# Optimization experiments

Measured on AMD Instinct MI355X. Metric: run time of the kernel, lower is better.

## Reference

```python
import jax, jax.numpy as jnp
import numpy as np

H = 1024        # bridge_hidden_dim
NH = 16         # num_attention_heads
HD = H // NH    # head_dim = 64
B, S = 4, 1024
PHYS_W = 0.2
CONS_W = 0.15


def setup_inputs() -> dict:
    key = jax.random.key(0)
    ks = jax.random.split(key, 16)
    sc = 0.02
    return {
        "cnn_features": jax.random.normal(ks[0], (B, S, H), jnp.float32),
        "llm_features": jax.random.normal(ks[1], (B, S, H), jnp.float32),
        "Wq": jax.random.normal(ks[2], (H, H), jnp.float32) * sc,
        "bq": jnp.zeros((H,), jnp.float32),
        "Wk": jax.random.normal(ks[3], (H, H), jnp.float32) * sc,
        "bk": jnp.zeros((H,), jnp.float32),
        "Wv": jax.random.normal(ks[4], (H, H), jnp.float32) * sc,
        "bv": jnp.zeros((H,), jnp.float32),
        "Wo": jax.random.normal(ks[5], (H, H), jnp.float32) * sc,
        "bo": jnp.zeros((H,), jnp.float32),
        "ln_g": jnp.ones((H,), jnp.float32),
        "ln_b": jnp.zeros((H,), jnp.float32),
        "e_energy": jax.random.normal(ks[6], (H,), jnp.float32),
        "e_mass": jax.random.normal(ks[7], (H,), jnp.float32),
        "e_momentum": jax.random.normal(ks[8], (H,), jnp.float32),
    }


def _layernorm(x, g, b, eps=1e-5):
    mu = jnp.mean(x, axis=-1, keepdims=True)
    var = jnp.var(x, axis=-1, keepdims=True)
    return (x - mu) * jax.lax.rsqrt(var + eps) * g + b


def _split_heads(x):
    b, s, _ = x.shape
    return x.reshape(b, s, NH, HD).transpose(0, 2, 1, 3)  # [b, h, s, d]


def _physics_attention(q_in, k_in, v_in, Wq, bq, Wk, bk, Wv, bv, Wo, bo, ln_g, ln_b):
    # q_in: [b, sq, H]; k_in == v_in: [b, sk, H] with sq == sk (required by bias math)
    Q = _split_heads(q_in @ Wq.T + bq)  # [b,h,s,d]
    K = _split_heads(k_in @ Wk.T + bk)
    V = _split_heads(v_in @ Wv.T + bv)
    scores = jnp.einsum('bhqd,bhkd->bhqk', Q, K) / jnp.sqrt(jnp.float32(HD))
    # physics constraints (broadcast [b,h,s,1] over key axis)
    energy_bias = jnp.sum(Q * K, axis=-1, keepdims=True) * PHYS_W
    mass_bias = jnp.mean(Q + K, axis=-1, keepdims=True) * CONS_W
    scores = scores + energy_bias + mass_bias
    attn = jax.nn.softmax(scores, axis=-1)  # dropout is identity in eval
    att = jnp.einsum('bhqk,bhkd->bhqd', attn, V)
    b, h, s, d = att.shape
    att = att.transpose(0, 2, 1, 3).reshape(b, s, h * d)
    out = att @ Wo.T + bo
    return _layernorm(q_in + out, ln_g, ln_b)


def reference(cnn_features, llm_features, Wq, bq, Wk, bk, Wv, bv, Wo, bo,
              ln_g, ln_b, e_energy, e_mass, e_momentum):
    b = cnn_features.shape[0]
    phys = jnp.stack([e_energy, e_mass, e_momentum], axis=0)  # [3, H]
    phys = jnp.broadcast_to(phys[None], (b, 3, H))
    aug_cnn = jnp.concatenate([cnn_features, phys], axis=1)  # [b, S+3, H]
    aug_llm = jnp.concatenate([llm_features, phys], axis=1)
    cnn_att = _physics_attention(aug_cnn, aug_llm, aug_llm,
                                 Wq, bq, Wk, bk, Wv, bv, Wo, bo, ln_g, ln_b)
    llm_att = _physics_attention(aug_llm, aug_cnn, aug_cnn,
                                 Wq, bq, Wk, bk, Wv, bv, Wo, bo, ln_g, ln_b)
    cnn_out = cnn_att[:, :cnn_features.shape[1], :]
    llm_out = llm_att[:, :llm_features.shape[1], :]
    return (cnn_out, llm_out)
```

## Files before the change

kernel.cpp:

```cpp
#include <hip/hip_runtime.h>
#include <stdint.h>

#define SA 1027
#define SPAD 1088

typedef __attribute__((ext_vector_type(8))) short short8;
typedef __attribute__((ext_vector_type(4))) float f32x4;
typedef __attribute__((ext_vector_type(2))) unsigned int u32x2;

typedef const __attribute__((address_space(1))) uint8_t* gas1;
typedef __attribute__((address_space(3))) uint8_t* las3;

__device__ __forceinline__ void gload16(const void* g, void* l){
  __builtin_amdgcn_global_load_lds((gas1)g, (las3)l, 16, 0, 0);
}

__device__ __forceinline__ uint16_t f2bf(float f){
  uint32_t x = __builtin_bit_cast(uint32_t, f);
  x = (x + 0x7fffu + ((x >> 16) & 1u)) >> 16;
  return (uint16_t)x;
}
__device__ __forceinline__ float bf2f(uint16_t u){
  uint32_t x = ((uint32_t)u) << 16;
  return __builtin_bit_cast(float, x);
}

__device__ __forceinline__ f32x4 mfma16(short8 a, short8 b, f32x4 c){
  return __builtin_amdgcn_mfma_f32_16x16x32_bf16(a, b, c, 0, 0, 0);
}

#define QSCALE 0.18033688011112042f

__global__ __launch_bounds__(256) void prep_wb(
    const float* __restrict__ Wq, const float* __restrict__ Wk,
    const float* __restrict__ Wv, const float* __restrict__ Wo,
    const float* __restrict__ bq, const float* __restrict__ bk,
    const float* __restrict__ bv, const float* __restrict__ bo,
    uint16_t* __restrict__ W, float* __restrict__ bias){
  const int gid = blockIdx.x*256 + threadIdx.x;
  if (gid < 1048576){
    const int w = gid >> 18;
    const int off = (gid & 262143) << 2;
    const float* src = (w==0) ? Wq : (w==1) ? Wk : (w==2) ? Wv : Wo;
    const float4 v = *(const float4*)(src + off);
    ushort4 u;
    u.x = f2bf(v.x); u.y = f2bf(v.y); u.z = f2bf(v.z); u.w = f2bf(v.w);
    *(ushort4*)(W + ((size_t)w << 20) + off) = u;
  } else if (gid < 1048576 + 1024){
    const int i = (gid - 1048576) << 2;
    const int w = i >> 10;
    const int off = i & 1023;
    const float* src = (w==0) ? bq : (w==1) ? bk : (w==2) ? bv : bo;
    *(float4*)(bias + i) = *(const float4*)(src + off);
  }
}

__global__ __launch_bounds__(256) void prep_X(
    const float* __restrict__ cnn, const float* __restrict__ llm,
    uint16_t* __restrict__ X){
  const int row = blockIdx.x;
  const int c4 = threadIdx.x << 2;
  const int cb = row >> 10, s = row & 1023;
  const int c = cb >> 2, b = cb & 3;
  const float4 v = *(const float4*)((c ? llm : cnn) + ((size_t)(b*1024 + s))*1024 + c4);
  ushort4 u;
  u.x = f2bf(v.x); u.y = f2bf(v.y); u.z = f2bf(v.z); u.w = f2bf(v.w);
  *(ushort4*)(X + (size_t)row*1024 + c4) = u;
}

__global__ __launch_bounds__(256) void phys_qkv(
    const float* __restrict__ ee, const float* __restrict__ em,
    const float* __restrict__ ep, const uint16_t* __restrict__ W,
    const float* __restrict__ bias, uint16_t* __restrict__ Yqk,
    uint16_t* __restrict__ Vt){
  __shared__ float xs[1024];
  const int t = blockIdx.x >> 3;
  const int col = 1024 + (blockIdx.x & 7)*256 + threadIdx.x;
  const float* e = (t==0) ? ee : (t==1) ? em : ep;
  for (int k = threadIdx.x; k < 1024; k += 256) xs[k] = bf2f(f2bf(e[k]));
  __syncthreads();
  const uint16_t* wr = W + (size_t)col*1024;
  float acc = 0.f;
  for (int k = 0; k < 1024; k += 8){
    const short8 w8 = *(const short8*)(wr + k);
    #pragma unroll
    for (int u = 0; u < 8; ++u) acc += bf2f((uint16_t)w8[u]) * xs[k+u];
  }
  const uint16_t o = f2bf(acc + bias[col]);
  if (col < 2048){
    #pragma unroll
    for (int cb = 0; cb < 8; ++cb)
      Yqk[((size_t)cb*SA + 1024 + t)*2048 + col] = o;
  } else {
    const int hd = col - 2048;
    #pragma unroll
    for (int cb = 0; cb < 8; ++cb)
      Vt[((size_t)(cb*1024 + hd))*SPAD + 1024 + t] = o;
  }
}

__global__ __launch_bounds__(512) void qkv256(
    const uint16_t* __restrict__ A, const uint16_t* __restrict__ B,
    const float* __restrict__ bias, uint16_t* __restrict__ Yqk,
    uint16_t* __restrict__ Vt){
  extern __shared__ uint8_t lds[];
  const int tid = threadIdx.x;
  const int lane = tid & 63, wid = tid >> 6;
  const int l15 = lane & 15, l4 = lane >> 4;
  const int wm = wid >> 2, wn = wid & 3;
  const int wg = (blockIdx.x & 7)*48 + (blockIdx.x >> 3);
  const int bm = wg / 12, bn = wg % 12;

  const uint16_t* Ag = A + (size_t)bm*256*1024;
  const uint16_t* Bg = B + (size_t)bn*256*1024;

  const int srow8 = lane >> 3;
  const int gch = (lane & 7) ^ srow8;
  const int c0 = wid*2, c1 = c0 + 1;
  const size_t ga0 = (size_t)(c0*8 + srow8)*1024 + gch*8;
  const size_t ga1 = (size_t)(c1*8 + srow8)*1024 + gch*8;

#define STG_A(buf, H, kt) do { \
    gload16(Ag + (size_t)(H)*131072 + (size_t)(kt)*64 + ga0, lds + (buf)*65536 + (H)*16384 + c0*1024); \
    gload16(Ag + (size_t)(H)*131072 + (size_t)(kt)*64 + ga1, lds + (buf)*65536 + (H)*16384 + c1*1024); \
  } while(0)
#define STG_B(buf, H, kt) do { \
    gload16(Bg + (size_t)(H)*131072 + (size_t)(kt)*64 + ga0, lds + (buf)*65536 + 32768 + (H)*16384 + c0*1024); \
    gload16(Bg + (size_t)(H)*131072 + (size_t)(kt)*64 + ga1, lds + (buf)*65536 + 32768 + (H)*16384 + c1*1024); \
  } while(0)

  int koff[2];
  koff[0] = (l4*16) ^ ((l15 & 7) << 4);
  koff[1] = (64 + l4*16) ^ ((l15 & 7) << 4);
  const int arow = (wm*128 + l15) * 128;
  const int brow = (wn*64 + l15) * 128;

  f32x4 acc[8][4];
  #pragma unroll
  for (int i = 0; i < 8; ++i)
    #pragma unroll
    for (int j = 0; j < 4; ++j) acc[i][j] = (f32x4){0.f,0.f,0.f,0.f};

  const int NT = 16;
  STG_A(0,0,0); STG_A(0,1,0); STG_B(0,0,0); STG_B(0,1,0);
  STG_B(1,0,1); STG_B(1,1,1);
  asm volatile("s_waitcnt vmcnt(4)" ::: "memory");
  __builtin_amdgcn_s_barrier();

  for (int s = 0; s < NT; ++s){
    const int b = s & 1;
    const uint8_t* La = lds + b*65536;
    const uint8_t* Lb = La + 32768;
    const int sn1 = (s+1 < NT) ? s+1 : s;
    const int sn2 = (s+2 < NT) ? s+2 : s;
    const int nb = b ^ 1;
    short8 af[4][2], bf0[2][2], bf1[2][2];

    STG_A(nb, 0, sn1);
    #pragma unroll
    for (int i = 0; i < 4; ++i){
      af[i][0] = *(const short8*)(La + arow + i*2048 + koff[0]);
      af[i][1] = *(const short8*)(La + arow + i*2048 + koff[1]);
    }
    #pragma unroll
    for (int j = 0; j < 2; ++j){
      bf0[j][0] = *(const short8*)(Lb + brow + j*2048 + koff[0]);
      bf0[j][1] = *(const short8*)(Lb + brow + j*2048 + koff[1]);
    }
    __builtin_amdgcn_s_barrier();
    asm volatile("s_waitcnt lgkmcnt(0)" ::: "memory");
    __builtin_amdgcn_s_setprio(1);
    #pragma unroll
    for (int i = 0; i < 4; ++i)
      #pragma unroll
      for (int j = 0; j < 2; ++j)
        acc[i][j] = mfma16(af[i][1], bf0[j][1], mfma16(af[i][0], bf0[j][0], acc[i][j]));
    __builtin_amdgcn_s_setprio(0);
    __builtin_amdgcn_s_barrier();

    STG_A(nb, 1, sn1);
    #pragma unroll
    for (int j = 0; j < 2; ++j){
      bf1[j][0] = *(const short8*)(Lb + brow + (j+2)*2048 + koff[0]);
      bf1[j][1] = *(const short8*)(Lb + brow + (j+2)*2048 + koff[1]);
    }
    __builtin_amdgcn_s_barrier();
    asm volatile("s_waitcnt lgkmcnt(0)" ::: "memory");
    __builtin_amdgcn_s_setprio(1);
    #pragma unroll
    for (int i = 0; i < 4; ++i)
      #pragma unroll
      for (int j = 0; j < 2; ++j)
        acc[i][j+2] = mfma16(af[i][1], bf1[j][1], mfma16(af[i][0], bf1[j][0], acc[i][j+2]));
    __builtin_amdgcn_s_setprio(0);
    __builtin_amdgcn_s_barrier();

    STG_B(b, 0, sn2);
    #pragma unroll
    for (int i = 0; i < 4; ++i){
      af[i][0] = *(const short8*)(La + 8192 + arow + i*2048 + koff[0]);
      af[i][1] = *(const short8*)(La + 8192 + arow + i*2048 + koff[1]);
    }
    __builtin_amdgcn_s_barrier();
    asm volatile("s_waitcnt lgkmcnt(0)" ::: "memory");
    __builtin_amdgcn_s_setprio(1);
    #pragma unroll
    for (int i = 0; i < 4; ++i)
      #pragma unroll
      for (int j = 0; j < 2; ++j)
        acc[i+4][j+2] = mfma16(af[i][1], bf1[j][1], mfma16(af[i][0], bf1[j][0], acc[i+4][j+2]));
    __builtin_amdgcn_s_setprio(0);
    __builtin_amdgcn_s_barrier();

    STG_B(b, 1, sn2);
    __builtin_amdgcn_s_barrier();
    __builtin_amdgcn_s_setprio(1);
    #pragma unroll
    for (int i = 0; i < 4; ++i)
      #pragma unroll
      for (int j = 0; j < 2; ++j)
        acc[i+4][j] = mfma16(af[i][1], bf0[j][1], mfma16(af[i][0], bf0[j][0], acc[i+4][j]));
    __builtin_amdgcn_s_setprio(0);
    asm volatile("s_waitcnt vmcnt(4)" ::: "memory");
    __builtin_amdgcn_s_barrier();
  }

  #pragma unroll
  for (int j = 0; j < 4; ++j){
    const int n = bn*256 + wn*64 + j*16 + l15;
    const float bb = bias[n];
    if (n < 2048){
      const float sc = (n < 1024) ? QSCALE : 1.0f;
      #pragma unroll
      for (int i = 0; i < 8; ++i){
        const int m0 = bm*256 + wm*128 + i*16 + l4*4;
        #pragma unroll
        for (int r = 0; r < 4; ++r){
          const int m = m0 + r;
          Yqk[((size_t)(m >> 10)*SA + (m & 1023))*2048 + n] = f2bf((acc[i][j][r] + bb) * sc);
        }
      }
    } else {
      const int hd = n - 2048;
      #pragma unroll
      for (int i = 0; i < 8; ++i){
        const int m0 = bm*256 + wm*128 + i*16 + l4*4;
        const size_t vrow = (size_t)(m0 >> 10)*1024 + hd;
        const uint32_t w0 = (uint32_t)f2bf(acc[i][j][0] + bb) | ((uint32_t)f2bf(acc[i][j][1] + bb) << 16);
        const uint32_t w1 = (uint32_t)f2bf(acc[i][j][2] + bb) | ((uint32_t)f2bf(acc[i][j][3] + bb) << 16);
        *(u32x2*)(Vt + vrow*SPAD + (m0 & 1023)) = (u32x2){w0, w1};
      }
    }
  }
#undef STG_A
#undef STG_B
}

__global__ __launch_bounds__(512) void oproj256(
    const uint16_t* __restrict__ A, const uint16_t* __restrict__ B,
    const float* __restrict__ bias, uint16_t* __restrict__ C){
  extern __shared__ uint8_t lds[];
  const int tid = threadIdx.x;
  const int lane = tid & 63, wid = tid >> 6;
  const int l15 = lane & 15, l4 = lane >> 4;
  const int wm = wid >> 2, wn = wid & 3;
  const int wg = (blockIdx.x & 7)*32 + (blockIdx.x >> 3);
  const int bm = wg >> 3, bn = wg & 7;

  const uint16_t* Ag = A + (size_t)bm*256*1024;
  const uint16_t* Bg = B + (size_t)bn*128*1024;

  const int srow8 = lane >> 3;
  const int gch = (lane & 7) ^ srow8;
  const int c0 = wid*2, c1 = c0 + 1;
  const size_t ga0 = (size_t)(c0*8 + srow8)*1024 + gch*8;
  const size_t ga1 = (size_t)(c1*8 + srow8)*1024 + gch*8;

#define STG_A(buf, H, kt) do { \
    gload16(Ag + (size_t)(H)*131072 + (size_t)(kt)*64 + ga0, lds + (buf)*49152 + (H)*16384 + c0*1024); \
    gload16(Ag + (size_t)(H)*131072 + (size_t)(kt)*64 + ga1, lds + (buf)*49152 + (H)*16384 + c1*1024); \
  } while(0)
#define STG_B(buf, kt) do { \
    gload16(Bg + (size_t)(kt)*64 + ga0, lds + (buf)*49152 + 32768 + c0*1024); \
    gload16(Bg + (size_t)(kt)*64 + ga1, lds + (buf)*49152 + 32768 + c1*1024); \
  } while(0)

  int koff[2];
  koff[0] = (l4*16) ^ ((l15 & 7) << 4);
  koff[1] = (64 + l4*16) ^ ((l15 & 7) << 4);
  const int abase = wm*16384 + l15*128;
  const int bbase = 32768 + (wn*32 + l15)*128;

  f32x4 acc[8][2];
  #pragma unroll
  for (int i = 0; i < 8; ++i){ acc[i][0] = (f32x4){0,0,0,0}; acc[i][1] = (f32x4){0,0,0,0}; }

  const int NT = 16;
  STG_A(0,0,0); STG_A(0,1,0); STG_B(0,0); STG_B(1,1);
  asm volatile("s_waitcnt vmcnt(2)" ::: "memory");
  __builtin_amdgcn_s_barrier();

  for (int s = 0; s < NT; ++s){
    const int b = s & 1, nb = b ^ 1;
    const uint8_t* L = lds + b*49152;
    const int sn1 = (s+1 < NT) ? s+1 : s;
    const int sn2 = (s+2 < NT) ? s+2 : s;
    short8 af[4][2], bfr[2][2];

    STG_A(nb, 0, sn1);
    #pragma unroll
    for (int i = 0; i < 4; ++i){
      af[i][0] = *(const short8*)(L + abase + i*2048 + koff[0]);
      af[i][1] = *(const short8*)(L + abase + i*2048 + koff[1]);
    }
    #pragma unroll
    for (int j = 0; j < 2; ++j){
      bfr[j][0] = *(const short8*)(L + bbase + j*2048 + koff[0]);
      bfr[j][1] = *(const short8*)(L + bbase + j*2048 + koff[1]);
    }
    __builtin_amdgcn_s_barrier();
    asm volatile("s_waitcnt lgkmcnt(0)" ::: "memory");
    __builtin_amdgcn_s_setprio(1);
    #pragma unroll
    for (int i = 0; i < 4; ++i)
      #pragma unroll
      for (int j = 0; j < 2; ++j)
        acc[i][j] = mfma16(af[i][1], bfr[j][1], mfma16(af[i][0], bfr[j][0], acc[i][j]));
    __builtin_amdgcn_s_setprio(0);
    __builtin_amdgcn_s_barrier();

    STG_A(nb, 1, sn1);
    STG_B(b, sn2);
    #pragma unroll
    for (int i = 0; i < 4; ++i){
      af[i][0] = *(const short8*)(L + abase + 8192 + i*2048 + koff[0]);
      af[i][1] = *(const short8*)(L + abase + 8192 + i*2048 + koff[1]);
    }
    __builtin_amdgcn_s_barrier();
    asm volatile("s_waitcnt lgkmcnt(0)" ::: "memory");
    __builtin_amdgcn_s_setprio(1);
    #pragma unroll
    for (int i = 0; i < 4; ++i)
      #pragma unroll
      for (int j = 0; j < 2; ++j)
        acc[i+4][j] = mfma16(af[i][1], bfr[j][1], mfma16(af[i][0], bfr[j][0], acc[i+4][j]));
    __builtin_amdgcn_s_setprio(0);
    asm volatile("s_waitcnt vmcnt(2)" ::: "memory");
    __builtin_amdgcn_s_barrier();
  }

  #pragma unroll
  for (int j = 0; j < 2; ++j){
    const int n = bn*128 + wn*32 + j*16 + l15;
    const float bb = bias[n];
    #pragma unroll
    for (int i = 0; i < 8; ++i){
      const size_t m0 = (size_t)bm*256 + wm*128 + i*16 + l4*4;
      #pragma unroll
      for (int r = 0; r < 4; ++r)
        C[(m0 + r)*1024 + n] = f2bf(acc[i][j][r] + bb);
    }
  }
#undef STG_A
#undef STG_B
}

__global__ __launch_bounds__(512, 4) void attn_k(
    const uint16_t* __restrict__ Yqk, const uint16_t* __restrict__ Vt,
    uint16_t* __restrict__ att){
  __shared__ __align__(16) uint8_t smK[16384];
  __shared__ __align__(16) uint8_t smV[16384];
  __shared__ __align__(16) uint8_t smP[16384];
  const int tid = threadIdx.x;
  const int lane = tid & 63, wid = tid >> 6;
  const int l15 = lane & 15, l4 = lane >> 4;
  const int i = blockIdx.x;
  const int inst = (i & 7)*16 + ((i >> 3) & 15);
  const int qb = i >> 7;
  const int h = inst & 15, cb = inst >> 4;
  const size_t yrow0 = (size_t)cb * SA;
  const int q0 = qb*256 + wid*32;
  const size_t vbase = (size_t)inst * 64 * SPAD;
  const uint16_t* Yk = Yqk + yrow0*2048 + 1024 + h*64;

  short8 qf[2][2];
  #pragma unroll
  for (int u = 0; u < 2; ++u){
    const uint16_t* p = Yqk + (yrow0 + q0 + u*16 + l15)*2048 + h*64 + l4*8;
    qf[u][0] = *(const short8*)p;
    qf[u][1] = *(const short8*)(p + 32);
  }

  f32x4 o0[4], o1[4];
  float psum0 = 0.f, psum1 = 0.f;
  #pragma unroll
  for (int d = 0; d < 4; ++d){ o0[d] = (f32x4){0,0,0,0}; o1[d] = (f32x4){0,0,0,0}; }

  int koff[2], pwo[4];
  #pragma unroll
  for (int kk = 0; kk < 2; ++kk)
    koff[kk] = (l15*128 + kk*64 + l4*16) ^ ((l15 & 7) << 4);
  #pragma unroll
  for (int nt = 0; nt < 4; ++nt)
    pwo[nt] = (l15*128 + nt*32 + l4*8) ^ ((l15 & 7) << 4);
  uint8_t* const pb = smP + wid*2048;

  const int srow = lane >> 3, schunk = lane & 7;
  const int strow = wid*8 + srow;
  const int sgch = schunk ^ srow;
  {
    gload16(Yk + (size_t)strow*2048 + sgch*8, smK + wid*1024);
    gload16(Vt + vbase + (size_t)strow*SPAD + sgch*8, smV + wid*1024);
  }
  __syncthreads();

  int cur = 0;
  for (int kt = 0; kt < 17; ++kt){
    if (kt < 16){
      const int s1n = (kt + 1)*64;
      const int nb = (cur ^ 1)*8192;
      gload16(Yk + (size_t)(s1n + strow)*2048 + sgch*8, smK + nb + wid*1024);
      gload16(Vt + vbase + (size_t)strow*SPAD + s1n + sgch*8, smV + nb + wid*1024);
    }
    const uint8_t* bK = smK + cur*8192;
    const uint8_t* bV = smV + cur*8192;

    f32x4 sa[4], sb[4];
    #pragma unroll
    for (int nt = 0; nt < 4; ++nt){
      const short8 k0 = *(const short8*)(bK + nt*2048 + koff[0]);
      const short8 k1 = *(const short8*)(bK + nt*2048 + koff[1]);
      sa[nt] = mfma16(k1, qf[0][1], mfma16(k0, qf[0][0], (f32x4){0,0,0,0}));
      sb[nt] = mfma16(k1, qf[1][1], mfma16(k0, qf[1][0], (f32x4){0,0,0,0}));
    }
    if (kt == 16){
      #pragma unroll
      for (int nt = 0; nt < 4; ++nt)
        #pragma unroll
        for (int r = 0; r < 4; ++r){
          if (nt*16 + l4*4 + r >= 3){ sa[nt][r] = -3e38f; sb[nt][r] = -3e38f; }
        }
    }
    #pragma unroll
    for (int nt = 0; nt < 4; ++nt){
      const float p0 = __builtin_amdgcn_exp2f(sa[nt][0]);
      const float p1 = __builtin_amdgcn_exp2f(sa[nt][1]);
      const float p2 = __builtin_amdgcn_exp2f(sa[nt][2]);
      const float p3 = __builtin_amdgcn_exp2f(sa[nt][3]);
      psum0 += (p0 + p1) + (p2 + p3);
      uint32_t w0, w1;
      asm("v_cvt_pk_bf16_f32 %0, %1, %2" : "=v"(w0) : "v"(p0), "v"(p1));
      asm("v_cvt_pk_bf16_f32 %0, %1, %2" : "=v"(w1) : "v"(p2), "v"(p3));
      *(u32x2*)(pb + pwo[nt]) = (u32x2){w0, w1};
    }
    short8 vf[4][2];
    #pragma unroll
    for (int dt = 0; dt < 4; ++dt){
      vf[dt][0] = *(const short8*)(bV + dt*2048 + koff[0]);
      vf[dt][1] = *(const short8*)(bV + dt*2048 + koff[1]);
    }
    #pragma unroll
    for (int kk = 0; kk < 2; ++kk){
      const short8 pf = *(const short8*)(pb + koff[kk]);
      #pragma unroll
      for (int dt = 0; dt < 4; ++dt)
        o0[dt] = mfma16(pf, vf[dt][kk], o0[dt]);
    }
    #pragma unroll
    for (int nt = 0; nt < 4; ++nt){
      const float p0 = __builtin_amdgcn_exp2f(sb[nt][0]);
      const float p1 = __builtin_amdgcn_exp2f(sb[nt][1]);
      const float p2 = __builtin_amdgcn_exp2f(sb[nt][2]);
      const float p3 = __builtin_amdgcn_exp2f(sb[nt][3]);
      psum1 += (p0 + p1) + (p2 + p3);
      uint32_t w0, w1;
      asm("v_cvt_pk_bf16_f32 %0, %1, %2" : "=v"(w0) : "v"(p0), "v"(p1));
      asm("v_cvt_pk_bf16_f32 %0, %1, %2" : "=v"(w1) : "v"(p2), "v"(p3));
      *(u32x2*)(pb + pwo[nt]) = (u32x2){w0, w1};
    }
    #pragma unroll
    for (int kk = 0; kk < 2; ++kk){
      const short8 pf = *(const short8*)(pb + koff[kk]);
      #pragma unroll
      for (int dt = 0; dt < 4; ++dt)
        o1[dt] = mfma16(pf, vf[dt][kk], o1[dt]);
    }
    __syncthreads();
    cur ^= 1;
  }

  psum0 += __shfl_xor(psum0, 16); psum0 += __shfl_xor(psum0, 32);
  psum1 += __shfl_xor(psum1, 16); psum1 += __shfl_xor(psum1, 32);
  const size_t arow0 = (size_t)cb*1024 + q0;
  #pragma unroll
  for (int r = 0; r < 4; ++r){
    const float inv0 = 1.f / __shfl(psum0, l4*4 + r);
    const float inv1 = 1.f / __shfl(psum1, l4*4 + r);
    #pragma unroll
    for (int dt = 0; dt < 4; ++dt){
      att[(arow0 + l4*4 + r)*1024 + h*64 + dt*16 + l15] = f2bf(o0[dt][r] * inv0);
      att[(arow0 + 16 + l4*4 + r)*1024 + h*64 + dt*16 + l15] = f2bf(o1[dt][r] * inv1);
    }
  }
}

__global__ __launch_bounds__(256) void ln_out(
    const uint16_t* __restrict__ Op, const float* __restrict__ cnn,
    const float* __restrict__ llm, const float* __restrict__ g,
    const float* __restrict__ b, float* __restrict__ out){
  const int row = blockIdx.x;
  const int c = row >> 12, bq = row & 4095;
  const int tid = threadIdx.x;
  const ushort4 u = *(const ushort4*)(Op + (size_t)row*1024 + (tid<<2));
  const float4 rv = *(const float4*)((c ? llm : cnn) + (size_t)bq*1024 + (tid<<2));
  const float x0 = bf2f(u.x) + rv.x;
  const float x1 = bf2f(u.y) + rv.y;
  const float x2 = bf2f(u.z) + rv.z;
  const float x3 = bf2f(u.w) + rv.w;
  float s1 = x0+x1+x2+x3;
  float s2 = x0*x0+x1*x1+x2*x2+x3*x3;
  #pragma unroll
  for (int m=1;m<64;m<<=1){ s1 += __shfl_xor(s1,m); s2 += __shfl_xor(s2,m); }
  __shared__ float r1[4], r2[4];
  const int wid = tid >> 6, lane = tid & 63;
  if (lane == 0){ r1[wid] = s1; r2[wid] = s2; }
  __syncthreads();
  s1 = r1[0]+r1[1]+r1[2]+r1[3];
  s2 = r2[0]+r2[1]+r2[2]+r2[3];
  const float mu = s1 * 0.0009765625f;
  const float var = s2 * 0.0009765625f - mu*mu;
  const float rs = rsqrtf(var + 1e-5f);
  const float4 gv = *(const float4*)(g + (tid<<2));
  const float4 bv = *(const float4*)(b + (tid<<2));
  float4 ov;
  ov.x = (x0 - mu)*rs*gv.x + bv.x;
  ov.y = (x1 - mu)*rs*gv.y + bv.y;
  ov.z = (x2 - mu)*rs*gv.z + bv.z;
  ov.w = (x3 - mu)*rs*gv.w + bv.w;
  *(float4*)(out + ((size_t)c << 22) + (size_t)bq*1024 + (tid<<2)) = ov;
}

extern "C" void kernel_launch(void* const* d_in, const int* in_sizes, int n_in,
                              void* d_out, int out_size, void* d_ws, size_t ws_size,
                              hipStream_t stream){
  const float* cnn = (const float*)d_in[0];
  const float* llm = (const float*)d_in[1];
  const float* Wq  = (const float*)d_in[2];
  const float* bq  = (const float*)d_in[3];
  const float* Wk  = (const float*)d_in[4];
  const float* bk  = (const float*)d_in[5];
  const float* Wv  = (const float*)d_in[6];
  const float* bv  = (const float*)d_in[7];
  const float* Wo  = (const float*)d_in[8];
  const float* bo  = (const float*)d_in[9];
  const float* lng = (const float*)d_in[10];
  const float* lnb = (const float*)d_in[11];
  const float* ee  = (const float*)d_in[12];
  const float* em  = (const float*)d_in[13];
  const float* ep  = (const float*)d_in[14];

  uint8_t* ws = (uint8_t*)d_ws;
  uint16_t* X    = (uint16_t*)(ws + 0);
  uint16_t* W    = (uint16_t*)(ws + 16777216);
  float*    bias = (float*)   (ws + 25165824);
  uint16_t* Yqk  = (uint16_t*)(ws + 25182208);
  uint16_t* Vt   = (uint16_t*)(ws + 59785216);
  uint16_t* att  = X;
  uint16_t* Op   = Yqk;
  float* out = (float*)d_out;

  hipFuncSetAttribute((const void*)qkv256,
                      hipFuncAttributeMaxDynamicSharedMemorySize, 131072);
  hipFuncSetAttribute((const void*)oproj256,
                      hipFuncAttributeMaxDynamicSharedMemorySize, 98304);

  prep_wb<<<4100, 256, 0, stream>>>(Wq, Wk, Wv, Wo, bq, bk, bv, bo, W, bias);
  prep_X<<<8192, 256, 0, stream>>>(cnn, llm, X);
  phys_qkv<<<24, 256, 0, stream>>>(ee, em, ep, W, bias, Yqk, Vt);
  qkv256<<<384, 512, 131072, stream>>>(X, W, bias, Yqk, Vt);
  attn_k<<<512, 512, 0, stream>>>(Yqk, Vt, att);
  oproj256<<<256, 512, 98304, stream>>>(att, W + 3145728, bias + 3072, Op);
  ln_out<<<8192, 256, 0, stream>>>(Op, cnn, llm, lng, lnb, out);
}
```

Measured before the change: 185.9 us.

## Deepen prefetch pipelines in GEMMs and attention, widen prep_X vector stores

The two GEMM kernels now prefetch whole A and B tiles two k-steps ahead at the end of each iteration, instead of interleaving next-buffer loads through the iteration, and wait on larger vmcnt counts. The attention kernel moves from double-buffered to triple-buffered K/V staging in dynamic LDS. It replaces the per-tile __syncthreads with a vmcnt wait plus barrier and pads the P scratch rows to 144 bytes in place of the XOR swizzle. prep_X handles 8 elements per thread with 16-byte stores across half as many blocks. The aim is to hide global-load latency behind MFMA work, at the cost of more LDS use and more complex waitcnt logic.

```diff
diff --git a/kernel.cpp b/kernel.cpp
--- a/kernel.cpp
+++ b/kernel.cpp
@@ -58,14 +58,17 @@
 __global__ __launch_bounds__(256) void prep_X(
     const float* __restrict__ cnn, const float* __restrict__ llm,
     uint16_t* __restrict__ X){
-  const int row = blockIdx.x;
-  const int c4 = threadIdx.x << 2;
+  const int row = blockIdx.x*2 + (threadIdx.x >> 7);
+  const int c8 = (threadIdx.x & 127) << 3;
   const int cb = row >> 10, s = row & 1023;
   const int c = cb >> 2, b = cb & 3;
-  const float4 v = *(const float4*)((c ? llm : cnn) + ((size_t)(b*1024 + s))*1024 + c4);
-  ushort4 u;
-  u.x = f2bf(v.x); u.y = f2bf(v.y); u.z = f2bf(v.z); u.w = f2bf(v.w);
-  *(ushort4*)(X + (size_t)row*1024 + c4) = u;
+  const float* src = (c ? llm : cnn) + ((size_t)(b*1024 + s))*1024 + c8;
+  const float4 v0 = *(const float4*)src;
+  const float4 v1 = *(const float4*)(src + 4);
+  short8 u;
+  u[0]=(short)f2bf(v0.x); u[1]=(short)f2bf(v0.y); u[2]=(short)f2bf(v0.z); u[3]=(short)f2bf(v0.w);
+  u[4]=(short)f2bf(v1.x); u[5]=(short)f2bf(v1.y); u[6]=(short)f2bf(v1.z); u[7]=(short)f2bf(v1.w);
+  *(short8*)(X + (size_t)row*1024 + c8) = u;
 }
 
 __global__ __launch_bounds__(256) void phys_qkv(
@@ -143,20 +146,16 @@
 
   const int NT = 16;
   STG_A(0,0,0); STG_A(0,1,0); STG_B(0,0,0); STG_B(0,1,0);
-  STG_B(1,0,1); STG_B(1,1,1);
-  asm volatile("s_waitcnt vmcnt(4)" ::: "memory");
+  STG_A(1,0,1); STG_A(1,1,1); STG_B(1,0,1); STG_B(1,1,1);
+  asm volatile("s_waitcnt vmcnt(8)" ::: "memory");
   __builtin_amdgcn_s_barrier();
 
   for (int s = 0; s < NT; ++s){
     const int b = s & 1;
     const uint8_t* La = lds + b*65536;
     const uint8_t* Lb = La + 32768;
-    const int sn1 = (s+1 < NT) ? s+1 : s;
-    const int sn2 = (s+2 < NT) ? s+2 : s;
-    const int nb = b ^ 1;
     short8 af[4][2], bf0[2][2], bf1[2][2];
 
-    STG_A(nb, 0, sn1);
     #pragma unroll
     for (int i = 0; i < 4; ++i){
       af[i][0] = *(const short8*)(La + arow + i*2048 + koff[0]);
@@ -178,7 +177,6 @@
     __builtin_amdgcn_s_setprio(0);
     __builtin_amdgcn_s_barrier();
 
-    STG_A(nb, 1, sn1);
     #pragma unroll
     for (int j = 0; j < 2; ++j){
       bf1[j][0] = *(const short8*)(Lb + brow + (j+2)*2048 + koff[0]);
@@ -195,12 +193,12 @@
     __builtin_amdgcn_s_setprio(0);
     __builtin_amdgcn_s_barrier();
 
-    STG_B(b, 0, sn2);
     #pragma unroll
     for (int i = 0; i < 4; ++i){
       af[i][0] = *(const short8*)(La + 8192 + arow + i*2048 + koff[0]);
       af[i][1] = *(const short8*)(La + 8192 + arow + i*2048 + koff[1]);
     }
+    if (s <= NT-3){ STG_B(b, 0, s+2); STG_B(b, 1, s+2); }
     __builtin_amdgcn_s_barrier();
     asm volatile("s_waitcnt lgkmcnt(0)" ::: "memory");
     __builtin_amdgcn_s_setprio(1);
@@ -212,7 +210,7 @@
     __builtin_amdgcn_s_setprio(0);
     __builtin_amdgcn_s_barrier();
 
-    STG_B(b, 1, sn2);
+    if (s <= NT-3){ STG_A(b, 0, s+2); STG_A(b, 1, s+2); }
     __builtin_amdgcn_s_barrier();
     __builtin_amdgcn_s_setprio(1);
     #pragma unroll
@@ -221,7 +219,8 @@
       for (int j = 0; j < 2; ++j)
         acc[i+4][j] = mfma16(af[i][1], bf0[j][1], mfma16(af[i][0], bf0[j][0], acc[i+4][j]));
     __builtin_amdgcn_s_setprio(0);
-    asm volatile("s_waitcnt vmcnt(4)" ::: "memory");
+    if (s <= NT-3)      asm volatile("s_waitcnt vmcnt(8)" ::: "memory");
+    else if (s == NT-2) asm volatile("s_waitcnt vmcnt(0)" ::: "memory");
     __builtin_amdgcn_s_barrier();
   }
 
@@ -296,56 +295,67 @@
   for (int i = 0; i < 8; ++i){ acc[i][0] = (f32x4){0,0,0,0}; acc[i][1] = (f32x4){0,0,0,0}; }
 
   const int NT = 16;
-  STG_A(0,0,0); STG_A(0,1,0); STG_B(0,0); STG_B(1,1);
-  asm volatile("s_waitcnt vmcnt(2)" ::: "memory");
+  STG_A(0,0,0); STG_A(0,1,0); STG_B(0,0);
+  STG_A(1,0,1); STG_A(1,1,1); STG_B(1,1);
+  asm volatile("s_waitcnt vmcnt(6)" ::: "memory");
   __builtin_amdgcn_s_barrier();
 
   for (int s = 0; s < NT; ++s){
-    const int b = s & 1, nb = b ^ 1;
+    const int b = s & 1;
     const uint8_t* L = lds + b*49152;
-    const int sn1 = (s+1 < NT) ? s+1 : s;
-    const int sn2 = (s+2 < NT) ? s+2 : s;
-    short8 af[4][2], bfr[2][2];
-
-    STG_A(nb, 0, sn1);
+    short8 af[4][2], af2[4][2], bfr[2][2];
+
     #pragma unroll
     for (int i = 0; i < 4; ++i){
       af[i][0] = *(const short8*)(L + abase + i*2048 + koff[0]);
       af[i][1] = *(const short8*)(L + abase + i*2048 + koff[1]);
     }
-    #pragma unroll
-    for (int j = 0; j < 2; ++j){
-      bfr[j][0] = *(const short8*)(L + bbase + j*2048 + koff[0]);
-      bfr[j][1] = *(const short8*)(L + bbase + j*2048 + koff[1]);
-    }
+    bfr[0][0] = *(const short8*)(L + bbase + koff[0]);
+    bfr[0][1] = *(const short8*)(L + bbase + koff[1]);
     __builtin_amdgcn_s_barrier();
     asm volatile("s_waitcnt lgkmcnt(0)" ::: "memory");
     __builtin_amdgcn_s_setprio(1);
     #pragma unroll
     for (int i = 0; i < 4; ++i)
-      #pragma unroll
-      for (int j = 0; j < 2; ++j)
-        acc[i][j] = mfma16(af[i][1], bfr[j][1], mfma16(af[i][0], bfr[j][0], acc[i][j]));
-    __builtin_amdgcn_s_setprio(0);
-    __builtin_amdgcn_s_barrier();
-
-    STG_A(nb, 1, sn1);
-    STG_B(b, sn2);
+      acc[i][0] = mfma16(af[i][1], bfr[0][1], mfma16(af[i][0], bfr[0][0], acc[i][0]));
+    __builtin_amdgcn_s_setprio(0);
+    __builtin_amdgcn_s_barrier();
+
+    bfr[1][0] = *(const short8*)(L + bbase + 2048 + koff[0]);
+    bfr[1][1] = *(const short8*)(L + bbase + 2048 + koff[1]);
+    __builtin_amdgcn_s_barrier();
+    asm volatile("s_waitcnt lgkmcnt(0)" ::: "memory");
+    __builtin_amdgcn_s_setprio(1);
+    #pragma unroll
+    for (int i = 0; i < 4; ++i)
+      acc[i][1] = mfma16(af[i][1], bfr[1][1], mfma16(af[i][0], bfr[1][0], acc[i][1]));
+    __builtin_amdgcn_s_setprio(0);
+    __builtin_amdgcn_s_barrier();
+
     #pragma unroll
     for (int i = 0; i < 4; ++i){
-      af[i][0] = *(const short8*)(L + abase + 8192 + i*2048 + koff[0]);
-      af[i][1] = *(const short8*)(L + abase + 8192 + i*2048 + koff[1]);
-    }
+      af2[i][0] = *(const short8*)(L + abase + 8192 + i*2048 + koff[0]);
+      af2[i][1] = *(const short8*)(L + abase + 8192 + i*2048 + koff[1]);
+    }
+    if (s <= NT-3){ STG_B(b, s+2); }
     __builtin_amdgcn_s_barrier();
     asm volatile("s_waitcnt lgkmcnt(0)" ::: "memory");
     __builtin_amdgcn_s_setprio(1);
     #pragma unroll
     for (int i = 0; i < 4; ++i)
-      #pragma unroll
-      for (int j = 0; j < 2; ++j)
-        acc[i+4][j] = mfma16(af[i][1], bfr[j][1], mfma16(af[i][0], bfr[j][0], acc[i+4][j]));
-    __builtin_amdgcn_s_setprio(0);
-    asm volatile("s_waitcnt vmcnt(2)" ::: "memory");
+      acc[i+4][1] = mfma16(af2[i][1], bfr[1][1], mfma16(af2[i][0], bfr[1][0], acc[i+4][1]));
+    __builtin_amdgcn_s_setprio(0);
+    __builtin_amdgcn_s_barrier();
+
+    if (s <= NT-3){ STG_A(b, 0, s+2); STG_A(b, 1, s+2); }
+    __builtin_amdgcn_s_barrier();
+    __builtin_amdgcn_s_setprio(1);
+    #pragma unroll
+    for (int i = 0; i < 4; ++i)
+      acc[i+4][0] = mfma16(af2[i][1], bfr[0][1], mfma16(af2[i][0], bfr[0][0], acc[i+4][0]));
+    __builtin_amdgcn_s_setprio(0);
+    if (s <= NT-3)      asm volatile("s_waitcnt vmcnt(6)" ::: "memory");
+    else if (s == NT-2) asm volatile("s_waitcnt vmcnt(0)" ::: "memory");
     __builtin_amdgcn_s_barrier();
   }
 
@@ -368,9 +378,7 @@
 __global__ __launch_bounds__(512, 4) void attn_k(
     const uint16_t* __restrict__ Yqk, const uint16_t* __restrict__ Vt,
     uint16_t* __restrict__ att){
-  __shared__ __align__(16) uint8_t smK[16384];
-  __shared__ __align__(16) uint8_t smV[16384];
-  __shared__ __align__(16) uint8_t smP[16384];
+  extern __shared__ uint8_t lds[];
   const int tid = threadIdx.x;
   const int lane = tid & 63, wid = tid >> 6;
   const int l15 = lane & 15, l4 = lane >> 4;
@@ -396,34 +404,36 @@
   #pragma unroll
   for (int d = 0; d < 4; ++d){ o0[d] = (f32x4){0,0,0,0}; o1[d] = (f32x4){0,0,0,0}; }
 
-  int koff[2], pwo[4];
-  #pragma unroll
-  for (int kk = 0; kk < 2; ++kk)
-    koff[kk] = (l15*128 + kk*64 + l4*16) ^ ((l15 & 7) << 4);
+  int koff[2], koffp[2], pwo[4];
+  #pragma unroll
+  for (int kk = 0; kk < 2; ++kk){
+    koff[kk]  = (l15*128 + kk*64 + l4*16) ^ ((l15 & 7) << 4);
+    koffp[kk] = l15*144 + kk*64 + l4*16;
+  }
   #pragma unroll
   for (int nt = 0; nt < 4; ++nt)
-    pwo[nt] = (l15*128 + nt*32 + l4*8) ^ ((l15 & 7) << 4);
-  uint8_t* const pb = smP + wid*2048;
+    pwo[nt] = l15*144 + nt*32 + l4*8;
+  uint8_t* const pb = lds + 49152 + wid*2304;
 
   const int srow = lane >> 3, schunk = lane & 7;
   const int strow = wid*8 + srow;
   const int sgch = schunk ^ srow;
-  {
-    gload16(Yk + (size_t)strow*2048 + sgch*8, smK + wid*1024);
-    gload16(Vt + vbase + (size_t)strow*SPAD + sgch*8, smV + wid*1024);
-  }
-  __syncthreads();
-
-  int cur = 0;
+
+#define ASTAGE(t3, kt) do { \
+    gload16(Yk + (size_t)((kt)*64 + strow)*2048 + sgch*8, lds + (t3)*8192 + wid*1024); \
+    gload16(Vt + vbase + (size_t)strow*SPAD + (kt)*64 + sgch*8, lds + 24576 + (t3)*8192 + wid*1024); \
+  } while(0)
+
+  ASTAGE(0, 0);
+  ASTAGE(1, 1);
+  asm volatile("s_waitcnt vmcnt(2)" ::: "memory");
+  __builtin_amdgcn_s_barrier();
+
   for (int kt = 0; kt < 17; ++kt){
-    if (kt < 16){
-      const int s1n = (kt + 1)*64;
-      const int nb = (cur ^ 1)*8192;
-      gload16(Yk + (size_t)(s1n + strow)*2048 + sgch*8, smK + nb + wid*1024);
-      gload16(Vt + vbase + (size_t)strow*SPAD + s1n + sgch*8, smV + nb + wid*1024);
-    }
-    const uint8_t* bK = smK + cur*8192;
-    const uint8_t* bV = smV + cur*8192;
+    const int c3 = kt % 3;
+    if (kt <= 14){ const int t3 = (kt + 2) % 3; ASTAGE(t3, kt + 2); }
+    const uint8_t* bK = lds + c3*8192;
+    const uint8_t* bV = lds + 24576 + c3*8192;
 
     f32x4 sa[4], sb[4];
     #pragma unroll
@@ -461,7 +471,7 @@
     }
     #pragma unroll
     for (int kk = 0; kk < 2; ++kk){
-      const short8 pf = *(const short8*)(pb + koff[kk]);
+      const short8 pf = *(const short8*)(pb + koffp[kk]);
       #pragma unroll
       for (int dt = 0; dt < 4; ++dt)
         o0[dt] = mfma16(pf, vf[dt][kk], o0[dt]);
@@ -480,14 +490,16 @@
     }
     #pragma unroll
     for (int kk = 0; kk < 2; ++kk){
-      const short8 pf = *(const short8*)(pb + koff[kk]);
+      const short8 pf = *(const short8*)(pb + koffp[kk]);
       #pragma unroll
       for (int dt = 0; dt < 4; ++dt)
         o1[dt] = mfma16(pf, vf[dt][kk], o1[dt]);
     }
-    __syncthreads();
-    cur ^= 1;
-  }
+    if (kt <= 14)      asm volatile("s_waitcnt vmcnt(2)" ::: "memory");
+    else if (kt == 15) asm volatile("s_waitcnt vmcnt(0)" ::: "memory");
+    if (kt <= 15) __builtin_amdgcn_s_barrier();
+  }
+#undef ASTAGE
 
   psum0 += __shfl_xor(psum0, 16); psum0 += __shfl_xor(psum0, 32);
   psum1 += __shfl_xor(psum1, 16); psum1 += __shfl_xor(psum1, 32);
@@ -573,12 +585,14 @@
                       hipFuncAttributeMaxDynamicSharedMemorySize, 131072);
   hipFuncSetAttribute((const void*)oproj256,
                       hipFuncAttributeMaxDynamicSharedMemorySize, 98304);
+  hipFuncSetAttribute((const void*)attn_k,
+                      hipFuncAttributeMaxDynamicSharedMemorySize, 67584);
 
   prep_wb<<<4100, 256, 0, stream>>>(Wq, Wk, Wv, Wo, bq, bk, bv, bo, W, bias);
-  prep_X<<<8192, 256, 0, stream>>>(cnn, llm, X);
+  prep_X<<<4096, 256, 0, stream>>>(cnn, llm, X);
   phys_qkv<<<24, 256, 0, stream>>>(ee, em, ep, W, bias, Yqk, Vt);
   qkv256<<<384, 512, 131072, stream>>>(X, W, bias, Yqk, Vt);
-  attn_k<<<512, 512, 0, stream>>>(Yqk, Vt, att);
+  attn_k<<<512, 512, 67584, stream>>>(Yqk, Vt, att);
   oproj256<<<256, 512, 98304, stream>>>(att, W + 3145728, bias + 3072, Op);
   ln_out<<<8192, 256, 0, stream>>>(Op, cnn, llm, lng, lnb, out);
 }
```

After: 189.8 us. 1.02x slower.
